# Performance work log

Hardware: AMD Instinct MI355X
Metric: run time of the kernel (lower is better)

## Reference

```python
import jax, jax.numpy as jnp
import numpy as np

D_MODEL = 1024
N_HEADS = 16
D_K = D_MODEL // N_HEADS


def setup_inputs() -> dict:
    key = jax.random.key(0)
    ks = jax.random.split(key, 12)
    B, S = 2, 2048
    scale = 1.0 / np.sqrt(D_MODEL)
    inp = {
        "q": jax.random.normal(ks[0], (B, S, D_MODEL), jnp.float32),
        "k": jax.random.normal(ks[1], (B, S, D_MODEL), jnp.float32),
        "v": jax.random.normal(ks[2], (B, S, D_MODEL), jnp.float32),
        "Wq": jax.random.normal(ks[3], (D_MODEL, D_MODEL), jnp.float32) * scale,
        "bq": jnp.zeros((D_MODEL,), jnp.float32),
        "Wk": jax.random.normal(ks[4], (D_MODEL, D_MODEL), jnp.float32) * scale,
        "bk": jnp.zeros((D_MODEL,), jnp.float32),
        "Wv": jax.random.normal(ks[5], (D_MODEL, D_MODEL), jnp.float32) * scale,
        "bv": jnp.zeros((D_MODEL,), jnp.float32),
        "Wo": jax.random.normal(ks[6], (D_MODEL, D_MODEL), jnp.float32) * scale,
        "bo": jnp.zeros((D_MODEL,), jnp.float32),
    }
    return inp


def reference(q, k, v, Wq, bq, Wk, bk, Wv, bv, Wo, bo):
    B, S, _ = q.shape
    # QKV projections, split into heads: [B, H, S, d_k]
    def proj(x, W, b):
        y = x @ W.T + b
        return y.reshape(B, -1, N_HEADS, D_K).transpose(0, 2, 1, 3)

    qh = proj(q, Wq, bq)
    kh = proj(k, Wk, bk)
    vh = proj(v, Wv, bv)

    scores = jnp.einsum("bhqd,bhkd->bhqk", qh, kh) / jnp.sqrt(
        jnp.asarray(D_K, qh.dtype)
    )
    attention = jax.nn.softmax(scores, axis=-1)  # dropout is identity in eval
    out = jnp.einsum("bhqk,bhkd->bhqd", attention, vh)
    out = out.transpose(0, 2, 1, 3).reshape(B, -1, N_HEADS * D_K)
    out = out @ Wo.T + bo
    return (out, attention)
```

## Files before the change

kernel.cpp:

```cpp
#include <hip/hip_runtime.h>

typedef __attribute__((ext_vector_type(4))) float f32x4;
typedef __attribute__((ext_vector_type(4))) unsigned short u16x4;
typedef __attribute__((ext_vector_type(8))) unsigned short u16x8;
typedef __attribute__((ext_vector_type(8))) short short8;
typedef __attribute__((ext_vector_type(4))) unsigned int u32x4;

#define DEVFN static __device__ __forceinline__

DEVFN unsigned short f2bf(float f) {
    union { float f; unsigned int u; } v; v.f = f;
    unsigned int r = v.u + 0x7FFFu + ((v.u >> 16) & 1u);
    return (unsigned short)(r >> 16);
}

DEVFN f32x4 mfma16(short8 a, short8 b, f32x4 c) {
    return __builtin_amdgcn_mfma_f32_16x16x32_bf16(a, b, c, 0, 0, 0);
}


__global__ __launch_bounds__(256) void cvt_w4(
    const float* __restrict__ w0, const float* __restrict__ w1,
    const float* __restrict__ w2, const float* __restrict__ w3,
    unsigned short* __restrict__ d0, unsigned short* __restrict__ d1,
    unsigned short* __restrict__ d2, unsigned short* __restrict__ d3) {
    const int z = blockIdx.y;
    const float* s = (z == 0) ? w0 : (z == 1) ? w1 : (z == 2) ? w2 : w3;
    unsigned short* d = (z == 0) ? d0 : (z == 1) ? d1 : (z == 2) ? d2 : d3;
    int i = (blockIdx.x * 256 + threadIdx.x) * 4;
    f32x4 v = *(const f32x4*)(s + i);
    u16x4 o;
    o[0] = f2bf(v[0]); o[1] = f2bf(v[1]); o[2] = f2bf(v[2]); o[3] = f2bf(v[3]);
    *(u16x4*)(d + i) = o;
}

__global__ __launch_bounds__(256) void qkv_gemm(
    const float* __restrict__ q, const float* __restrict__ k, const float* __restrict__ v,
    const unsigned short* __restrict__ Wqb, const unsigned short* __restrict__ Wkb,
    const unsigned short* __restrict__ Wvb,
    const float* __restrict__ bq, const float* __restrict__ bk, const float* __restrict__ bv,
    unsigned short* __restrict__ qh, unsigned short* __restrict__ kh,
    unsigned short* __restrict__ vt)
{
    constexpr int AS = 40;
    __shared__ __attribute__((aligned(16))) unsigned short Asm[128 * AS];
    __shared__ __attribute__((aligned(16))) unsigned short Bsm[128 * AS];

    const int z = blockIdx.y;
    const float* X = (z == 0) ? q : (z == 1) ? k : v;
    const unsigned short* W = (z == 0) ? Wqb : (z == 1) ? Wkb : Wvb;
    const float* bias = (z == 0) ? bq : (z == 1) ? bk : bv;

    const int bid0 = blockIdx.x;
    const int swz = (bid0 & 7) * 32 + (bid0 >> 3);
    const int bm = swz >> 3, bn = swz & 7;

    const int tid = threadIdx.x;
    const int lane = tid & 63, wid = tid >> 6;
    const int wm = wid >> 1, wn = wid & 1;
    const int lg = lane >> 4, lr = lane & 15;

    f32x4 acc[4][4] = {};

    const float* Xb = X + (size_t)(bm * 128) * 1024;
    const unsigned short* Wb = W + (size_t)(bn * 128) * 1024;
    const int ar = tid >> 3, ac = (tid & 7) * 4;
    const int br = tid >> 2, bc = (tid & 3) * 8;

    for (int kt = 0; kt < 32; ++kt) {
        __syncthreads();
        #pragma unroll
        for (int s4 = 0; s4 < 4; ++s4) {
            int row = s4 * 32 + ar;
            f32x4 xv = *(const f32x4*)(Xb + (size_t)row * 1024 + kt * 32 + ac);
            u16x4 pk;
            pk[0] = f2bf(xv[0]); pk[1] = f2bf(xv[1]);
            pk[2] = f2bf(xv[2]); pk[3] = f2bf(xv[3]);
            *(u16x4*)(&Asm[row * AS + ac]) = pk;
        }
        #pragma unroll
        for (int s2 = 0; s2 < 2; ++s2) {
            int row = s2 * 64 + br;
            *(u16x8*)(&Bsm[row * AS + bc]) =
                *(const u16x8*)(Wb + (size_t)row * 1024 + kt * 32 + bc);
        }
        __syncthreads();

        short8 af[4], bf[4];
        #pragma unroll
        for (int i = 0; i < 4; i++)
            af[i] = *(const short8*)(&Asm[(wm * 64 + i * 16 + lr) * AS + lg * 8]);
        #pragma unroll
        for (int j = 0; j < 4; j++)
            bf[j] = *(const short8*)(&Bsm[(wn * 64 + j * 16 + lr) * AS + lg * 8]);

        if (z != 2) {
            #pragma unroll
            for (int i = 0; i < 4; i++)
                #pragma unroll
                for (int j = 0; j < 4; j++)
                    acc[i][j] = mfma16(af[i], bf[j], acc[i][j]);
        } else {
            #pragma unroll
            for (int i = 0; i < 4; i++)
                #pragma unroll
                for (int j = 0; j < 4; j++)
                    acc[i][j] = mfma16(bf[i], af[j], acc[i][j]);
        }
    }

    if (z != 2) {
        unsigned short* Y = (z == 0) ? qh : kh;
        #pragma unroll
        for (int i = 0; i < 4; i++) {
            int mrow = bm * 128 + wm * 64 + i * 16 + lg * 4;
            #pragma unroll
            for (int j = 0; j < 4; j++) {
                int ncol = bn * 128 + wn * 64 + j * 16 + lr;
                float bb = bias[ncol];
                #pragma unroll
                for (int ii = 0; ii < 4; ii++)
                    Y[(size_t)(mrow + ii) * 1024 + ncol] = f2bf(acc[i][j][ii] + bb);
            }
        }
    } else {
        #pragma unroll
        for (int i = 0; i < 4; i++) {
            int nrow0 = bn * 128 + wn * 64 + i * 16 + lg * 4;
            #pragma unroll
            for (int j = 0; j < 4; j++) {
                int mcol = bm * 128 + wm * 64 + j * 16 + lr;
                int b_ = mcol >> 11, s_ = mcol & 2047;
                #pragma unroll
                for (int ii = 0; ii < 4; ii++) {
                    int nrow = nrow0 + ii;
                    float val = acc[i][j][ii] + bias[nrow];
                    int h_ = nrow >> 6, d_ = nrow & 63;
                    vt[(size_t)((b_ * 16 + h_) * 64 + d_) * 2048 + s_] = f2bf(val);
                }
            }
        }
    }
}

__global__ __launch_bounds__(512, 4) void attn_fused(
    const unsigned short* __restrict__ qh,
    const unsigned short* __restrict__ kh,
    const unsigned short* __restrict__ vt,
    float* __restrict__ attn_out, unsigned short* __restrict__ ctx)
{
    __shared__ float Lsm[8][16];
    __shared__ float Om[8][1024];

    const int bid = blockIdx.x;
    const int swz = (bid & 7) * 512 + (bid >> 3);
    const int bh = swz >> 7, qt = swz & 127;
    const int b = bh >> 4, h = bh & 15;
    const int tid = threadIdx.x, ks = tid >> 6, lane = tid & 63;
    const int lg = lane >> 4, lr = lane & 15;
    const int qbase = qt * 16;

    const unsigned short* Qrow = qh + (size_t)(b * 2048 + qbase + lr) * 1024 + h * 64;
    short8 bq0 = *(const short8*)(Qrow + lg * 8);
    short8 bq1 = *(const short8*)(Qrow + 32 + lg * 8);

    const unsigned short* Kbase = kh + (size_t)(b * 2048 + ks * 256) * 1024 + h * 64;
    const unsigned short* Vbase = vt + (size_t)(bh * 64) * 2048 + ks * 256;

    const int a0 = lg & 1;
    const bool bswap = (lg == 1) || (lg == 2);

    unsigned int paw[4][8];
    float lsum = 0.f;

    #pragma unroll
    for (int kt = 0; kt < 4; ++kt) {
        f32x4 sc[4] = {};
        const unsigned short* Kt = Kbase + (size_t)(kt * 64) * 1024;
        #pragma unroll
        for (int c = 0; c < 4; c++) {
            const unsigned short* Kr = Kt + (size_t)(c * 16 + lr) * 1024 + lg * 8;
            sc[c] = mfma16(*(const short8*)(Kr), bq0, sc[c]);
            sc[c] = mfma16(*(const short8*)(Kr + 32), bq1, sc[c]);
        }
        float p[4][4];
        #pragma unroll
        for (int c = 0; c < 4; c++)
            #pragma unroll
            for (int i = 0; i < 4; i++) {
                p[c][i] = __expf(sc[c][i] * 0.125f);
                lsum += p[c][i];
            }

        unsigned int w32[4][2];
        #pragma unroll
        for (int c = 0; c < 4; c++)
            #pragma unroll
            for (int w = 0; w < 2; w++)
                asm("v_cvt_pk_bf16_f32 %0, %1, %2"
                    : "=v"(w32[c][w]) : "v"(p[c][2 * w]), "v"(p[c][2 * w + 1]));

        unsigned int Av[2][2][2];
        #pragma unroll
        for (int t = 0; t < 2; t++)
            #pragma unroll
            for (int w = 0; w < 2; w++) {
                unsigned int keep = a0 ? w32[2 * t + 1][w] : w32[2 * t][w];
                unsigned int snd  = a0 ? w32[2 * t][w]     : w32[2 * t + 1][w];
                unsigned int rcv = __shfl_xor(snd, 16, 64);
                Av[t][0][w] = a0 ? rcv : keep;
                Av[t][1][w] = a0 ? keep : rcv;
            }
        #pragma unroll
        for (int t = 0; t < 2; t++)
            #pragma unroll
            for (int s = 0; s < 2; s++)
                #pragma unroll
                for (int w = 0; w < 2; w++) {
                    unsigned int sw = __shfl_xor(Av[t][s][w], 48, 64);
                    paw[kt][t * 4 + s * 2 + w] = bswap ? sw : Av[t][s][w];
                }
    }

    lsum += __shfl_xor(lsum, 16, 64);
    lsum += __shfl_xor(lsum, 32, 64);
    if (lg == 0) Lsm[ks][lr] = lsum;
    __syncthreads();
    float Lt = 0.f;
    #pragma unroll
    for (int w = 0; w < 8; w++) Lt += Lsm[w][lr];
    const float il = 1.0f / Lt;

    f32x4 o[4] = {};
    #pragma unroll
    for (int kt = 0; kt < 4; ++kt) {
        u32x4 w0 = { paw[kt][0], paw[kt][1], paw[kt][2], paw[kt][3] };
        u32x4 w1 = { paw[kt][4], paw[kt][5], paw[kt][6], paw[kt][7] };
        short8 pa0 = *(short8*)&w0;
        short8 pa1 = *(short8*)&w1;

        const unsigned short* Vt = Vbase + kt * 64;
        #pragma unroll
        for (int g = 0; g < 4; g++) {
            const unsigned short* Vr = Vt + (size_t)(g * 16 + lr) * 2048 + lg * 8;
            o[g] = mfma16(pa0, *(const short8*)(Vr), o[g]);
            o[g] = mfma16(pa1, *(const short8*)(Vr + 32), o[g]);
        }
    }

    __syncthreads();
    {
        float* Ob = &Om[ks][0];
        #pragma unroll
        for (int g = 0; g < 4; g++)
            #pragma unroll
            for (int i = 0; i < 4; i++)
                Ob[(lg * 4 + i) * 64 + g * 16 + lr] = o[g][i];
    }
    __syncthreads();
    #pragma unroll
    for (int rr = 0; rr < 2; rr++) {
        int r = ks * 2 + rr;
        float Ls = 0.f;
        #pragma unroll
        for (int w = 0; w < 8; w++) Ls += Lsm[w][r];
        float s = 0.f;
        #pragma unroll
        for (int w = 0; w < 8; w++) s += Om[w][r * 64 + lane];
        ctx[(size_t)(b * 2048 + qbase + r) * 1024 + h * 64 + lane] = f2bf(s / Ls);
    }

    float* prow = attn_out + (size_t)(bh * 2048 + qbase + lr) * 2048 + ks * 256;
    #pragma unroll
    for (int kt = 0; kt < 4; ++kt) {
        float sl[8], sh[8];
        #pragma unroll
        for (int r = 0; r < 8; r++) {
            unsigned int u = paw[kt][r];
            sl[r] = __uint_as_float(u << 16) * il;
            sh[r] = __uint_as_float(u & 0xFFFF0000u) * il;
        }
        float* pk = prow + kt * 64 + lg * 8;
        f32x4 st0 = { sl[0], sh[0], sl[1], sh[1] };
        f32x4 st1 = { sl[2], sh[2], sl[3], sh[3] };
        f32x4 st2 = { sl[4], sh[4], sl[5], sh[5] };
        f32x4 st3 = { sl[6], sh[6], sl[7], sh[7] };
        *(f32x4*)(pk)      = st0;
        *(f32x4*)(pk + 4)  = st1;
        *(f32x4*)(pk + 32) = st2;
        *(f32x4*)(pk + 36) = st3;
    }
}

__global__ __launch_bounds__(256) void out_gemm(
    const unsigned short* __restrict__ ctx, const unsigned short* __restrict__ Wob,
    const float* __restrict__ bo, float* __restrict__ out)
{
    constexpr int AS = 40;
    __shared__ __attribute__((aligned(16))) unsigned short Asm[128 * AS];
    __shared__ __attribute__((aligned(16))) unsigned short Bsm[128 * AS];

    const int bid0 = blockIdx.x;
    const int swz = (bid0 & 7) * 32 + (bid0 >> 3);
    const int bm = swz >> 3, bn = swz & 7;
    const int tid = threadIdx.x;
    const int lane = tid & 63, wid = tid >> 6;
    const int wm = wid >> 1, wn = wid & 1;
    const int lg = lane >> 4, lr = lane & 15;

    f32x4 acc[4][4] = {};

    const unsigned short* Ab = ctx + (size_t)(bm * 128) * 1024;
    const unsigned short* Wb = Wob + (size_t)(bn * 128) * 1024;
    const int br = tid >> 2, bc = (tid & 3) * 8;

    for (int kt = 0; kt < 32; ++kt) {
        __syncthreads();
        #pragma unroll
        for (int s2 = 0; s2 < 2; ++s2) {
            int row = s2 * 64 + br;
            *(u16x8*)(&Asm[row * AS + bc]) =
                *(const u16x8*)(Ab + (size_t)row * 1024 + kt * 32 + bc);
            *(u16x8*)(&Bsm[row * AS + bc]) =
                *(const u16x8*)(Wb + (size_t)row * 1024 + kt * 32 + bc);
        }
        __syncthreads();

        short8 af[4], bf[4];
        #pragma unroll
        for (int i = 0; i < 4; i++)
            af[i] = *(const short8*)(&Asm[(wm * 64 + i * 16 + lr) * AS + lg * 8]);
        #pragma unroll
        for (int j = 0; j < 4; j++)
            bf[j] = *(const short8*)(&Bsm[(wn * 64 + j * 16 + lr) * AS + lg * 8]);
        #pragma unroll
        for (int i = 0; i < 4; i++)
            #pragma unroll
            for (int j = 0; j < 4; j++)
                acc[i][j] = mfma16(af[i], bf[j], acc[i][j]);
    }

    #pragma unroll
    for (int i = 0; i < 4; i++) {
        int mrow = bm * 128 + wm * 64 + i * 16 + lg * 4;
        #pragma unroll
        for (int j = 0; j < 4; j++) {
            int ncol = bn * 128 + wn * 64 + j * 16 + lr;
            float bb = bo[ncol];
            #pragma unroll
            for (int ii = 0; ii < 4; ii++)
                out[(size_t)(mrow + ii) * 1024 + ncol] = acc[i][j][ii] + bb;
        }
    }
}

extern "C" void kernel_launch(void* const* d_in, const int* in_sizes, int n_in,
                              void* d_out, int out_size, void* d_ws, size_t ws_size,
                              hipStream_t stream) {
    const float* q  = (const float*)d_in[0];
    const float* k  = (const float*)d_in[1];
    const float* v  = (const float*)d_in[2];
    const float* Wq = (const float*)d_in[3];
    const float* bq = (const float*)d_in[4];
    const float* Wk = (const float*)d_in[5];
    const float* bk = (const float*)d_in[6];
    const float* Wv = (const float*)d_in[7];
    const float* bv = (const float*)d_in[8];
    const float* Wo = (const float*)d_in[9];
    const float* bo = (const float*)d_in[10];

    float* out  = (float*)d_out;
    float* attn = out + (size_t)4096 * 1024;

    unsigned short* wsp = (unsigned short*)d_ws;
    unsigned short* Wqb = wsp;
    unsigned short* Wkb = wsp + (size_t)(1 << 20);
    unsigned short* Wvb = wsp + (size_t)2 * (1 << 20);
    unsigned short* Wob = wsp + (size_t)3 * (1 << 20);
    unsigned short* qh  = wsp + (size_t)4 * (1 << 20);
    unsigned short* kh  = wsp + (size_t)8 * (1 << 20);
    unsigned short* vt  = wsp + (size_t)12 * (1 << 20);
    unsigned short* ctx = wsp + (size_t)16 * (1 << 20);

    cvt_w4<<<dim3(1024, 4), 256, 0, stream>>>(Wq, Wk, Wv, Wo, Wqb, Wkb, Wvb, Wob);

    qkv_gemm<<<dim3(256, 3), 256, 0, stream>>>(q, k, v, Wqb, Wkb, Wvb,
                                               bq, bk, bv, qh, kh, vt);

    attn_fused<<<4096, 512, 0, stream>>>(qh, kh, vt, attn, ctx);

    out_gemm<<<256, 256, 0, stream>>>(ctx, Wob, bo, out);
}
```

Before: 467.3 us.

## Split attention probability write into separate recompute kernel

The fused attention kernel no longer writes the full probability matrix; it stores only the per-row inverse softmax denominators. A new kernel recomputes QK^T with MFMA, applies exp and normalisation, and streams the fp32 probabilities out with nontemporal stores. The aim is to take the large attention-matrix store off the register-heavy PV kernel and let a lighter kernel saturate write bandwidth, at the cost of recomputing the scores and an extra launch. The recompute applies exp without subtracting the row max, so it only matches the reference if the denominator was computed the same way and the scores stay in range.

```diff
diff --git a/kernel.cpp b/kernel.cpp
--- a/kernel.cpp
+++ b/kernel.cpp
@@ -143,11 +143,11 @@
     }
 }
 
-__global__ __launch_bounds__(512, 4) void attn_fused(
+__global__ __launch_bounds__(512, 4) void attn_pv(
     const unsigned short* __restrict__ qh,
     const unsigned short* __restrict__ kh,
     const unsigned short* __restrict__ vt,
-    float* __restrict__ attn_out, unsigned short* __restrict__ ctx)
+    float* __restrict__ Linv, unsigned short* __restrict__ ctx)
 {
     __shared__ float Lsm[8][16];
     __shared__ float Om[8][1024];
@@ -270,25 +270,54 @@
         ctx[(size_t)(b * 2048 + qbase + r) * 1024 + h * 64 + lane] = f2bf(s / Ls);
     }
 
-    float* prow = attn_out + (size_t)(bh * 2048 + qbase + lr) * 2048 + ks * 256;
-    #pragma unroll
-    for (int kt = 0; kt < 4; ++kt) {
-        float sl[8], sh[8];
-        #pragma unroll
-        for (int r = 0; r < 8; r++) {
-            unsigned int u = paw[kt][r];
-            sl[r] = __uint_as_float(u << 16) * il;
-            sh[r] = __uint_as_float(u & 0xFFFF0000u) * il;
-        }
-        float* pk = prow + kt * 64 + lg * 8;
-        f32x4 st0 = { sl[0], sh[0], sl[1], sh[1] };
-        f32x4 st1 = { sl[2], sh[2], sl[3], sh[3] };
-        f32x4 st2 = { sl[4], sh[4], sl[5], sh[5] };
-        f32x4 st3 = { sl[6], sh[6], sl[7], sh[7] };
-        *(f32x4*)(pk)      = st0;
-        *(f32x4*)(pk + 4)  = st1;
-        *(f32x4*)(pk + 32) = st2;
-        *(f32x4*)(pk + 36) = st3;
+    if (ks == 0 && lg == 0)
+        Linv[(size_t)bh * 2048 + qbase + lr] = il;
+}
+
+__global__ __launch_bounds__(256) void prob_write(
+    const unsigned short* __restrict__ qh,
+    const unsigned short* __restrict__ kh,
+    const float* __restrict__ Linv,
+    float* __restrict__ attn_out)
+{
+    const int bid = blockIdx.x;
+    const int swz = (bid & 7) * 128 + (bid >> 3);
+    const int bh = swz >> 5, qt = swz & 31;
+    const int b = bh >> 4, h = bh & 15;
+    const int tid = threadIdx.x, wid = tid >> 6, lane = tid & 63;
+    const int lg = lane >> 4, lr = lane & 15;
+    const int qrow0 = qt * 64 + wid * 16;
+
+    const unsigned short* Qrow = qh + (size_t)(b * 2048 + qrow0 + lr) * 1024 + h * 64;
+    short8 aq0 = *(const short8*)(Qrow + lg * 8);
+    short8 aq1 = *(const short8*)(Qrow + 32 + lg * 8);
+
+    float li[4];
+    #pragma unroll
+    for (int i = 0; i < 4; i++)
+        li[i] = Linv[(size_t)bh * 2048 + qrow0 + lg * 4 + i];
+
+    const unsigned short* Kbase = kh + (size_t)(b * 2048) * 1024 + h * 64;
+    float* Pout = attn_out + (size_t)(bh * 2048 + qrow0) * 2048;
+
+    #pragma unroll 1
+    for (int kt = 0; kt < 32; ++kt) {
+        f32x4 sc[4] = {};
+        const unsigned short* Kt = Kbase + (size_t)(kt * 64) * 1024;
+        #pragma unroll
+        for (int c = 0; c < 4; c++) {
+            const unsigned short* Kr = Kt + (size_t)(c * 16 + lr) * 1024 + lg * 8;
+            sc[c] = mfma16(aq0, *(const short8*)(Kr), sc[c]);
+            sc[c] = mfma16(aq1, *(const short8*)(Kr + 32), sc[c]);
+        }
+        #pragma unroll
+        for (int c = 0; c < 4; c++)
+            #pragma unroll
+            for (int i = 0; i < 4; i++) {
+                float p = __expf(sc[c][i] * 0.125f) * li[i];
+                __builtin_nontemporal_store(p,
+                    Pout + (size_t)(lg * 4 + i) * 2048 + kt * 64 + c * 16 + lr);
+            }
     }
 }
 
@@ -381,13 +410,16 @@
     unsigned short* kh  = wsp + (size_t)8 * (1 << 20);
     unsigned short* vt  = wsp + (size_t)12 * (1 << 20);
     unsigned short* ctx = wsp + (size_t)16 * (1 << 20);
+    float* Linv = (float*)(wsp + (size_t)20 * (1 << 20));
 
     cvt_w4<<<dim3(1024, 4), 256, 0, stream>>>(Wq, Wk, Wv, Wo, Wqb, Wkb, Wvb, Wob);
 
     qkv_gemm<<<dim3(256, 3), 256, 0, stream>>>(q, k, v, Wqb, Wkb, Wvb,
                                                bq, bk, bv, qh, kh, vt);
 
-    attn_fused<<<4096, 512, 0, stream>>>(qh, kh, vt, attn, ctx);
+    attn_pv<<<4096, 512, 0, stream>>>(qh, kh, vt, Linv, ctx);
+
+    prob_write<<<1024, 256, 0, stream>>>(qh, kh, Linv, attn);
 
     out_gemm<<<256, 256, 0, stream>>>(ctx, Wob, bo, out);
 }
```

Result: slower. 520.8 us (+11.4%).
